# Performance work log

Measured on AMD Instinct MI355X. Metric: run time of the kernel, lower is better.

## Reference

```python
import jax, jax.numpy as jnp
import numpy as np

B, N, C, K, COUT = 2, 16384, 64, 17, 128  # K = neighbors+self; kernel_size = K-1


def setup_inputs() -> dict:
    key = jax.random.key(0)
    kx, ka, kw = jax.random.split(key, 3)
    x = jax.random.normal(kx, (B, N, C), dtype=jnp.float32)
    # neighbor indices in [0, N), guaranteed != self via offset trick (avoids 0/0 in frame normalization)
    off = jax.random.randint(ka, (B, N, K), 1, N)
    adj = ((jnp.arange(N)[None, :, None] + off) % N).astype(jnp.int32)
    # kaiming_uniform-like init scale
    bound = 1.0 / np.sqrt(C * (K - 1))
    weight = jax.random.uniform(kw, (COUT, C, K - 1), dtype=jnp.float32, minval=-bound, maxval=bound)
    return {"x": x, "adj": adj, "weight": weight}


def reference(x, adj, weight):
    # x: [B,N,C], adj: [B,N,K] int, weight: [Cout,C,K-1]
    knn_idx = adj[:, :, 1:]                      # [B,N,K-1] drop self column
    knn = jax.vmap(lambda xb, ib: xb[ib])(x, knn_idx)   # gather -> [B,N,K-1,C]
    diff = knn - x[:, :, None, :]                # [B,N,K-1,C]
    norm = jnp.sqrt(jnp.sum(diff * diff, axis=-1, keepdims=True))   # [B,N,K-1,1]
    frame = jnp.concatenate([diff, norm], axis=-1)                  # [B,N,K-1,C+1]
    frame = frame / jnp.sqrt(jnp.sum(frame * frame, axis=-1, keepdims=True))
    radius = 1.0
    proj = radius * frame[..., :-1]              # drop norm coord -> [B,N,K-1,C]
    # per-neighbor kernel slice contraction, then ReLU and max over neighborhood
    out = jnp.einsum('ocj,bnjc->bonj', weight, proj)  # [B,Cout,N,K-1]
    out = jnp.max(jax.nn.relu(out), axis=-1)          # [B,Cout,N]
    return out
```

## Files before the change

kernel.cpp:

```cpp
#include <hip/hip_runtime.h>
#include <hip/hip_bf16.h>

typedef __attribute__((ext_vector_type(8))) short bf16x8;
typedef __attribute__((ext_vector_type(4))) float f32x4;

#define N_PTS   16384
#define C_CH    64
#define K_ADJ   17
#define C_OUT   128
#define N_J     16

__device__ __hip_bfloat16 g_wb[N_J * C_OUT * C_CH];

__global__ __launch_bounds__(256) void prep_weights_k(const float* __restrict__ w) {
    int idx = blockIdx.x * 256 + threadIdx.x;
    int p = idx & 63;
    int o = (idx >> 6) & 127;
    int j = idx >> 13;
    int hi = p >> 5, q = p & 31, la = q >> 3, r = q & 7;
    int c = hi * 32 + (r < 4 ? la * 4 + r : 16 + la * 4 + (r - 4));
    g_wb[idx] = __float2bfloat16(w[(o * C_CH + c) * (K_ADJ - 1) + j]);
}

__global__ __launch_bounds__(256) void sconv_k(
    const float* __restrict__ x,
    const int*   __restrict__ adj,
    float*       __restrict__ out)
{
    __shared__ __hip_bfloat16 lds_w[4 * C_OUT * C_CH];

    const int pblk = blockIdx.x;
    const int g8   = pblk & 7;
    const int b    = g8 >> 2;
    const int slot = ((pblk >> 3) << 2) | (g8 & 3);

    const int tid  = threadIdx.x;
    const int lane = tid & 63;
    const int wid  = tid >> 6;
    const int lrow = lane & 15;
    const int lk   = lane >> 4;

    const int n = slot * 64 + wid * 16 + lrow;

    const float* __restrict__ xb   = x   + (size_t)b * N_PTS * C_CH;
    const int*   __restrict__ adjb = adj + (size_t)b * N_PTS * K_ADJ;
    float*       __restrict__ ob   = out + (size_t)b * C_OUT * N_PTS;

    float ctr[16];
    {
        const float* rp = xb + (size_t)n * C_CH + lk * 4;
        #pragma unroll
        for (int i = 0; i < 4; ++i) {
            float4 v = *(const float4*)(rp + i * 16);
            ctr[i*4+0]=v.x; ctr[i*4+1]=v.y; ctr[i*4+2]=v.z; ctr[i*4+3]=v.w;
        }
    }

    int aidx[N_J];
    {
        const int base = n * K_ADJ + 1;
        #pragma unroll
        for (int j = 0; j < N_J; ++j) aidx[j] = adjb[base + j];
    }

    f32x4 maxacc[8];
    #pragma unroll
    for (int of = 0; of < 8; ++of) maxacc[of] = f32x4{0.f, 0.f, 0.f, 0.f};

    float4 q0, q1, q2, q3;
    {
        const float* gp = xb + (size_t)aidx[0] * C_CH + lk * 4;
        q0 = *(const float4*)(gp +  0);
        q1 = *(const float4*)(gp + 16);
        q2 = *(const float4*)(gp + 32);
        q3 = *(const float4*)(gp + 48);
    }

    for (int cch = 0; cch < 4; ++cch) {
        if (cch) __syncthreads();
        const __hip_bfloat16* gw = g_wb + cch * (4 * C_OUT * C_CH);
        #pragma unroll
        for (int it = 0; it < 16; ++it) {
            const int m   = tid + it * 256;
            const bf16x8 v = *(const bf16x8*)(gw + m * 8);
            const int row = m >> 3;
            const int c8s = (m & 7) ^ (row & 7);
            *(bf16x8*)&lds_w[(row * 8 + c8s) * 8] = v;
        }
        __syncthreads();

        #pragma unroll
        for (int jj = 0; jj < 4; ++jj) {
            const int j = cch * 4 + jj;

            float d[16];
            d[0]=q0.x;  d[1]=q0.y;  d[2]=q0.z;  d[3]=q0.w;
            d[4]=q1.x;  d[5]=q1.y;  d[6]=q1.z;  d[7]=q1.w;
            d[8]=q2.x;  d[9]=q2.y;  d[10]=q2.z; d[11]=q2.w;
            d[12]=q3.x; d[13]=q3.y; d[14]=q3.z; d[15]=q3.w;

            if (j < N_J - 1) {
                const float* gp = xb + (size_t)aidx[j + 1] * C_CH + lk * 4;
                q0 = *(const float4*)(gp +  0);
                q1 = *(const float4*)(gp + 16);
                q2 = *(const float4*)(gp + 32);
                q3 = *(const float4*)(gp + 48);
            }

            float s = 0.f;
            #pragma unroll
            for (int i = 0; i < 16; ++i) { d[i] -= ctr[i]; s = fmaf(d[i], d[i], s); }
            s += __shfl_xor(s, 16);
            s += __shfl_xor(s, 32);
            const float scale = rsqrtf(2.0f * s);

            bf16x8 bf0, bf1;
            #pragma unroll
            for (int i = 0; i < 8; ++i) {
                bf0[i] = (short)__builtin_bit_cast(unsigned short, __float2bfloat16(d[i]     * scale));
                bf1[i] = (short)__builtin_bit_cast(unsigned short, __float2bfloat16(d[i + 8] * scale));
            }

            const int sw = lrow & 7;
            #pragma unroll
            for (int of = 0; of < 8; ++of) {
                const int row = jj * 128 + of * 16 + lrow;
                const bf16x8 a0 = *(const bf16x8*)&lds_w[(row * 8 + ( lk      ^ sw)) * 8];
                const bf16x8 a1 = *(const bf16x8*)&lds_w[(row * 8 + ((4 + lk) ^ sw)) * 8];
                f32x4 acc = f32x4{0.f, 0.f, 0.f, 0.f};
                acc = __builtin_amdgcn_mfma_f32_16x16x32_bf16(a0, bf0, acc, 0, 0, 0);
                acc = __builtin_amdgcn_mfma_f32_16x16x32_bf16(a1, bf1, acc, 0, 0, 0);
                #pragma unroll
                for (int r = 0; r < 4; ++r)
                    maxacc[of][r] = fmaxf(maxacc[of][r], acc[r]);
            }
        }
    }

    #pragma unroll
    for (int of = 0; of < 8; ++of) {
        const int o0 = of * 16 + lk * 4;
        #pragma unroll
        for (int r = 0; r < 4; ++r)
            ob[(size_t)(o0 + r) * N_PTS + n] = maxacc[of][r];
    }
}

extern "C" void kernel_launch(void* const* d_in, const int* in_sizes, int n_in,
                              void* d_out, int out_size, void* d_ws, size_t ws_size,
                              hipStream_t stream) {
    (void)in_sizes; (void)n_in; (void)d_ws; (void)ws_size; (void)out_size;
    const float* x   = (const float*)d_in[0];
    const int*   adj = (const int*)d_in[1];
    const float* w   = (const float*)d_in[2];
    float*       out = (float*)d_out;

    hipLaunchKernelGGL(prep_weights_k, dim3(512), dim3(256), 0, stream, w);
    hipLaunchKernelGGL(sconv_k,        dim3(512), dim3(256), 0, stream, x, adj, out);
}
```

Baseline: 84.81 us.

## Double-buffer weight chunks in LDS via direct global-to-LDS loads, deeper gather prefetch

Weights are pre-swizzled in the prep kernel so the main kernel can copy them straight into LDS with global_load_lds into two buffers, refilling one buffer while the other is consumed. Blocks grow to 512 threads covering 128 points each, halving the grid so each weight load serves twice as many points. The neighbor-row gather now prefetches two neighbors ahead instead of one. The cost is double the LDS per block (64KB), which may cut occupancy, plus more registers held by the extra prefetch buffers.

```diff
diff --git a/kernel.cpp b/kernel.cpp
--- a/kernel.cpp
+++ b/kernel.cpp
@@ -14,20 +14,39 @@
 
 __global__ __launch_bounds__(256) void prep_weights_k(const float* __restrict__ w) {
     int idx = blockIdx.x * 256 + threadIdx.x;
-    int p = idx & 63;
-    int o = (idx >> 6) & 127;
-    int j = idx >> 13;
-    int hi = p >> 5, q = p & 31, la = q >> 3, r = q & 7;
-    int c = hi * 32 + (r < 4 ? la * 4 + r : 16 + la * 4 + (r - 4));
-    g_wb[idx] = __float2bfloat16(w[(o * C_CH + c) * (K_ADJ - 1) + j]);
+    int S   = idx >> 3, r = idx & 7;
+    int c   = S >> 12, s = S & 4095;
+    int row = s >> 3,  c8 = s & 7;
+    int p8  = c8 ^ (row & 7);
+    int j   = c * 4 + (row >> 7);
+    int o   = row & 127;
+    int p   = p8 * 8 + r;
+    int hi  = p >> 5, q = p & 31, la = q >> 3, rr = q & 7;
+    int ch  = hi * 32 + (rr < 4 ? la * 4 + rr : 16 + la * 4 + (rr - 4));
+    g_wb[idx] = __float2bfloat16(w[(o * C_CH + ch) * (K_ADJ - 1) + j]);
 }
 
-__global__ __launch_bounds__(256) void sconv_k(
+#define GLOAD(gp, lp) __builtin_amdgcn_global_load_lds(                       \
+    (const __attribute__((address_space(1))) void*)(gp),                      \
+    (__attribute__((address_space(3))) void*)(lp), 16, 0, 0)
+
+struct PF { float4 v0, v1, v2, v3; };
+
+__device__ __forceinline__ void issue_gather(PF& p, const float* __restrict__ xb,
+                                             int row, int lk) {
+    const float* gp = xb + (size_t)row * C_CH + lk * 4;
+    p.v0 = *(const float4*)(gp +  0);
+    p.v1 = *(const float4*)(gp + 16);
+    p.v2 = *(const float4*)(gp + 32);
+    p.v3 = *(const float4*)(gp + 48);
+}
+
+__global__ __launch_bounds__(512) void sconv_k(
     const float* __restrict__ x,
     const int*   __restrict__ adj,
     float*       __restrict__ out)
 {
-    __shared__ __hip_bfloat16 lds_w[4 * C_OUT * C_CH];
+    __shared__ __hip_bfloat16 lds_w[2][4 * C_OUT * C_CH];
 
     const int pblk = blockIdx.x;
     const int g8   = pblk & 7;
@@ -36,15 +55,22 @@
 
     const int tid  = threadIdx.x;
     const int lane = tid & 63;
-    const int wid  = tid >> 6;
+    const int w8   = tid >> 6;
     const int lrow = lane & 15;
     const int lk   = lane >> 4;
 
-    const int n = slot * 64 + wid * 16 + lrow;
+    const int n = slot * 128 + w8 * 16 + lrow;
 
     const float* __restrict__ xb   = x   + (size_t)b * N_PTS * C_CH;
     const int*   __restrict__ adjb = adj + (size_t)b * N_PTS * K_ADJ;
     float*       __restrict__ ob   = out + (size_t)b * C_OUT * N_PTS;
+
+    #pragma unroll
+    for (int i = 0; i < 8; ++i) {
+        const int lo = (w8 * 8 + i) * 512;
+        GLOAD(g_wb +     lo + lane * 8, &lds_w[0][lo]);
+        GLOAD(g_wb + 32768 + lo + lane * 8, &lds_w[1][lo]);
+    }
 
     float ctr[16];
     {
@@ -67,44 +93,33 @@
     #pragma unroll
     for (int of = 0; of < 8; ++of) maxacc[of] = f32x4{0.f, 0.f, 0.f, 0.f};
 
-    float4 q0, q1, q2, q3;
-    {
-        const float* gp = xb + (size_t)aidx[0] * C_CH + lk * 4;
-        q0 = *(const float4*)(gp +  0);
-        q1 = *(const float4*)(gp + 16);
-        q2 = *(const float4*)(gp + 32);
-        q3 = *(const float4*)(gp + 48);
-    }
+    PF pf0, pf1;
+    issue_gather(pf0, xb, aidx[0], lk);
+    issue_gather(pf1, xb, aidx[1], lk);
 
-    for (int cch = 0; cch < 4; ++cch) {
-        if (cch) __syncthreads();
-        const __hip_bfloat16* gw = g_wb + cch * (4 * C_OUT * C_CH);
-        #pragma unroll
-        for (int it = 0; it < 16; ++it) {
-            const int m   = tid + it * 256;
-            const bf16x8 v = *(const bf16x8*)(gw + m * 8);
-            const int row = m >> 3;
-            const int c8s = (m & 7) ^ (row & 7);
-            *(bf16x8*)&lds_w[(row * 8 + c8s) * 8] = v;
-        }
-        __syncthreads();
+    __syncthreads();
+
+    const int sw = lrow & 7;
+
+    #pragma unroll
+    for (int c = 0; c < 4; ++c) {
+        const __hip_bfloat16* buf = lds_w[c & 1];
 
         #pragma unroll
         for (int jj = 0; jj < 4; ++jj) {
-            const int j = cch * 4 + jj;
+            const int j = c * 4 + jj;
 
             float d[16];
-            d[0]=q0.x;  d[1]=q0.y;  d[2]=q0.z;  d[3]=q0.w;
-            d[4]=q1.x;  d[5]=q1.y;  d[6]=q1.z;  d[7]=q1.w;
-            d[8]=q2.x;  d[9]=q2.y;  d[10]=q2.z; d[11]=q2.w;
-            d[12]=q3.x; d[13]=q3.y; d[14]=q3.z; d[15]=q3.w;
-
-            if (j < N_J - 1) {
-                const float* gp = xb + (size_t)aidx[j + 1] * C_CH + lk * 4;
-                q0 = *(const float4*)(gp +  0);
-                q1 = *(const float4*)(gp + 16);
-                q2 = *(const float4*)(gp + 32);
-                q3 = *(const float4*)(gp + 48);
+            {
+                const PF& p = (j & 1) ? pf1 : pf0;
+                d[0] =p.v0.x; d[1] =p.v0.y; d[2] =p.v0.z; d[3] =p.v0.w;
+                d[4] =p.v1.x; d[5] =p.v1.y; d[6] =p.v1.z; d[7] =p.v1.w;
+                d[8] =p.v2.x; d[9] =p.v2.y; d[10]=p.v2.z; d[11]=p.v2.w;
+                d[12]=p.v3.x; d[13]=p.v3.y; d[14]=p.v3.z; d[15]=p.v3.w;
+            }
+            if (j + 2 < N_J) {
+                if (j & 1) issue_gather(pf1, xb, aidx[j + 2], lk);
+                else       issue_gather(pf0, xb, aidx[j + 2], lk);
             }
 
             float s = 0.f;
@@ -121,18 +136,26 @@
                 bf1[i] = (short)__builtin_bit_cast(unsigned short, __float2bfloat16(d[i + 8] * scale));
             }
 
-            const int sw = lrow & 7;
             #pragma unroll
             for (int of = 0; of < 8; ++of) {
                 const int row = jj * 128 + of * 16 + lrow;
-                const bf16x8 a0 = *(const bf16x8*)&lds_w[(row * 8 + ( lk      ^ sw)) * 8];
-                const bf16x8 a1 = *(const bf16x8*)&lds_w[(row * 8 + ((4 + lk) ^ sw)) * 8];
+                const bf16x8 a0 = *(const bf16x8*)&buf[(row * 8 + ( lk      ^ sw)) * 8];
+                const bf16x8 a1 = *(const bf16x8*)&buf[(row * 8 + ((4 + lk) ^ sw)) * 8];
                 f32x4 acc = f32x4{0.f, 0.f, 0.f, 0.f};
                 acc = __builtin_amdgcn_mfma_f32_16x16x32_bf16(a0, bf0, acc, 0, 0, 0);
                 acc = __builtin_amdgcn_mfma_f32_16x16x32_bf16(a1, bf1, acc, 0, 0, 0);
                 #pragma unroll
                 for (int r = 0; r < 4; ++r)
                     maxacc[of][r] = fmaxf(maxacc[of][r], acc[r]);
+            }
+        }
+
+        __syncthreads();
+        if (c < 2) {
+            #pragma unroll
+            for (int i = 0; i < 8; ++i) {
+                const int lo = (w8 * 8 + i) * 512;
+                GLOAD(g_wb + (c + 2) * 32768 + lo + lane * 8, &lds_w[c & 1][lo]);
             }
         }
     }
@@ -156,5 +179,5 @@
     float*       out = (float*)d_out;
 
     hipLaunchKernelGGL(prep_weights_k, dim3(512), dim3(256), 0, stream, w);
-    hipLaunchKernelGGL(sconv_k,        dim3(512), dim3(256), 0, stream, x, adj, out);
+    hipLaunchKernelGGL(sconv_k,        dim3(256), dim3(512), 0, stream, x, adj, out);
 }
```

New measurement: 90.29 us. 1.06x slower.
